# Kernel tuning notes

Measured on AMD Instinct MI355X. Metric: run time of the kernel, lower is better.

The kernel has to match this reference:

```python
import jax, jax.numpy as jnp
import numpy as np

N_NODES = 262144
MEM_DIM = 512
MSG_DIM = 1024
N_UPD = 65536


def setup_inputs() -> dict:
    key = jax.random.key(0)
    ks = jax.random.split(key, 8)
    memory = jax.random.normal(ks[0], (N_NODES, MEM_DIM), dtype=jnp.float32)
    last_update = jnp.zeros((N_NODES,), dtype=jnp.float32)
    # unique node ids (in-place scatter assumes no duplicates)
    node_ids = jax.random.permutation(ks[1], N_NODES)[:N_UPD].astype(jnp.int64)
    messages = jax.random.normal(ks[2], (N_UPD, MSG_DIM), dtype=jnp.float32)
    timestamps = jax.random.uniform(ks[3], (N_UPD,), dtype=jnp.float32)
    s_ih = 1.0 / np.sqrt(MEM_DIM)
    W_ih = jax.random.normal(ks[4], (3 * MEM_DIM, MSG_DIM), dtype=jnp.float32) * s_ih
    W_hh = jax.random.normal(ks[5], (3 * MEM_DIM, MEM_DIM), dtype=jnp.float32) * s_ih
    b_ih = jnp.zeros((3 * MEM_DIM,), dtype=jnp.float32)
    b_hh = jnp.zeros((3 * MEM_DIM,), dtype=jnp.float32)
    return {"memory": memory, "last_update": last_update, "node_ids": node_ids,
            "messages": messages, "timestamps": timestamps,
            "W_ih": W_ih, "W_hh": W_hh, "b_ih": b_ih, "b_hh": b_hh}


def gru_cell(x, h, W_ih, W_hh, b_ih, b_hh):
    # torch.nn.GRUCell semantics
    gi = x @ W_ih.T + b_ih  # [n, 3H]
    gh = h @ W_hh.T + b_hh  # [n, 3H]
    i_r, i_z, i_n = jnp.split(gi, 3, axis=-1)
    h_r, h_z, h_n = jnp.split(gh, 3, axis=-1)
    r = jax.nn.sigmoid(i_r + h_r)
    z = jax.nn.sigmoid(i_z + h_z)
    n = jnp.tanh(i_n + r * h_n)
    return (1.0 - z) * n + z * h


def reference(memory, last_update, node_ids, messages, timestamps, W_ih, W_hh, b_ih, b_hh):
    # get_updated_memory: gather -> GRU cell -> scatter back into a copy
    h = memory[node_ids]  # [n_upd, MEM_DIM]
    h_new = gru_cell(messages, h, W_ih, W_hh, b_ih, b_hh)
    updated_memory = memory.at[node_ids].set(h_new)
    updated_last_update = last_update.at[node_ids].set(timestamps)
    return updated_memory, updated_last_update
```

## Files before the change

kernel.cpp:

```cpp
#include <hip/hip_runtime.h>

#define N_NODES 262144
#define MEM_DIM 512
#define MSG_DIM 1024
#define N_UPD   65536

typedef __attribute__((ext_vector_type(8)))  __bf16 bf16x8;
typedef __attribute__((ext_vector_type(16))) float  floatx16;
typedef __attribute__((ext_vector_type(4)))  unsigned short ushortx4;

static __device__ __forceinline__ unsigned short f2bf(float f) {
  unsigned int u = __float_as_uint(f);
  u += 0x7fffu + ((u >> 16) & 1u);
  return (unsigned short)(u >> 16);
}

static __device__ __forceinline__ void async16(const void* g, void* l) {
  __builtin_amdgcn_global_load_lds(
      (const __attribute__((address_space(1))) unsigned int*)g,
      (__attribute__((address_space(3))) unsigned int*)l, 16, 0, 0);
}

__global__ void cvt_kernel(const float4* __restrict__ src,
                           ushortx4* __restrict__ dst, int n4) {
  int stride = gridDim.x * blockDim.x;
  for (int i = blockIdx.x * blockDim.x + threadIdx.x; i < n4; i += stride) {
    float4 v = src[i];
    ushortx4 o;
    o.x = f2bf(v.x); o.y = f2bf(v.y); o.z = f2bf(v.z); o.w = f2bf(v.w);
    dst[i] = o;
  }
}

__global__ void gather_cvt_kernel(const float* __restrict__ memory,
                                  const int* __restrict__ ids,
                                  ushortx4* __restrict__ dst) {
  int u = blockIdx.x * blockDim.x + threadIdx.x;
  int i = u >> 7, c4 = u & 127;
  int g = ids[i];
  const float4* row = (const float4*)(memory + (size_t)g * MEM_DIM);
  float4 v = row[c4];
  ushortx4 o;
  o.x = f2bf(v.x); o.y = f2bf(v.y); o.z = f2bf(v.z); o.w = f2bf(v.w);
  dst[u] = o;
}

__global__ void copy_kernel(const float4* __restrict__ mem,
                            const float4* __restrict__ lu,
                            float4* __restrict__ out_mem,
                            float4* __restrict__ out_lu) {
  const int NM4 = N_NODES * MEM_DIM / 4;
  const int NL4 = N_NODES / 4;
  int stride = gridDim.x * blockDim.x;
  for (int i = blockIdx.x * blockDim.x + threadIdx.x; i < NM4 + NL4; i += stride) {
    if (i < NM4) out_mem[i] = mem[i];
    else         out_lu[i - NM4] = lu[i - NM4];
  }
}

__global__ __launch_bounds__(256, 2)
void gru_kernel(const unsigned short* __restrict__ msgb,
                const unsigned short* __restrict__ hb,
                const unsigned short* __restrict__ wih,
                const unsigned short* __restrict__ whh,
                const float* __restrict__ b_ih, const float* __restrict__ b_hh,
                const float* __restrict__ memory,
                const int* __restrict__ ids,
                const float* __restrict__ ts,
                float* __restrict__ out_mem, float* __restrict__ out_lu) {
  __shared__ unsigned short sA[128 * 64];
  __shared__ unsigned short sB[192 * 64];

  const int tid  = threadIdx.x;
  const int lane = tid & 63;
  const int w    = tid >> 6;
  const int wm   = w & 1, wn = w >> 1;
  const int hc   = blockIdx.x * 64;
  const int m0   = blockIdx.y * 128;

  if (blockIdx.x == 0 && tid < 128) {
    int m = m0 + tid;
    out_lu[ids[m]] = ts[m];
  }

  floatx16 accR[2], accZ[2], accN[2][2];
#pragma unroll
  for (int t = 0; t < 2; ++t)
#pragma unroll
    for (int e = 0; e < 16; ++e) {
      accR[t][e] = 0.f; accZ[t][e] = 0.f;
      accN[0][t][e] = 0.f; accN[1][t][e] = 0.f;
    }

  const int srow = tid >> 3;
  const int scol = (tid & 7) * 8;
  const int lrow = lane & 31;
  const int lko  = (lane >> 5) * 8;

#pragma unroll
  for (int phase = 0; phase < 2; ++phase) {
    const unsigned short* Ap = phase ? hb : msgb;
    const unsigned short* Bp = phase ? whh : wih;
    const int K = phase ? 512 : 1024;
    for (int k0 = 0; k0 < K; k0 += 64) {
      __syncthreads();
#pragma unroll
      for (int j = 0; j < 4; ++j) {
        const unsigned short* g = Ap + (size_t)(m0 + j * 32 + srow) * K + (k0 + scol);
        async16(g, (char*)sA + j * 4096 + w * 1024);
      }
#pragma unroll
      for (int j = 0; j < 6; ++j) {
        int brr  = j * 32 + srow;
        int gate = brr >> 6;
        int wr   = gate * 512 + hc + (brr & 63);
        const unsigned short* g = Bp + (size_t)wr * K + (k0 + scol);
        async16(g, (char*)sB + j * 4096 + w * 1024);
      }
      __syncthreads();
#pragma unroll
      for (int kk = 0; kk < 4; ++kk) {
        int ko = kk * 16 + lko;
        bf16x8 a0 = *(const bf16x8*)&sA[(wm * 64 + lrow) * 64 + ko];
        bf16x8 a1 = *(const bf16x8*)&sA[(wm * 64 + 32 + lrow) * 64 + ko];
        bf16x8 vr = *(const bf16x8*)&sB[(wn * 32 + lrow) * 64 + ko];
        bf16x8 vz = *(const bf16x8*)&sB[(64 + wn * 32 + lrow) * 64 + ko];
        bf16x8 vn = *(const bf16x8*)&sB[(128 + wn * 32 + lrow) * 64 + ko];
        accR[0] = __builtin_amdgcn_mfma_f32_32x32x16_bf16(a0, vr, accR[0], 0, 0, 0);
        accR[1] = __builtin_amdgcn_mfma_f32_32x32x16_bf16(a1, vr, accR[1], 0, 0, 0);
        accZ[0] = __builtin_amdgcn_mfma_f32_32x32x16_bf16(a0, vz, accZ[0], 0, 0, 0);
        accZ[1] = __builtin_amdgcn_mfma_f32_32x32x16_bf16(a1, vz, accZ[1], 0, 0, 0);
        accN[phase][0] = __builtin_amdgcn_mfma_f32_32x32x16_bf16(a0, vn, accN[phase][0], 0, 0, 0);
        accN[phase][1] = __builtin_amdgcn_mfma_f32_32x32x16_bf16(a1, vn, accN[phase][1], 0, 0, 0);
      }
    }
  }

  const int col = hc + wn * 32 + lrow;
  const float biasR  = b_ih[col] + b_hh[col];
  const float biasZ  = b_ih[512 + col] + b_hh[512 + col];
  const float biasNi = b_ih[1024 + col];
  const float biasNh = b_hh[1024 + col];
#pragma unroll
  for (int t = 0; t < 2; ++t) {
#pragma unroll
    for (int r = 0; r < 16; ++r) {
      int rowin = (r & 3) + 8 * (r >> 2) + 4 * (lane >> 5);
      int m = m0 + wm * 64 + t * 32 + rowin;
      int g = ids[m];
      size_t off = (size_t)g * MEM_DIM + col;
      float h  = memory[off];
      float rr = __builtin_amdgcn_rcpf(1.f + __expf(-(accR[t][r] + biasR)));
      float zz = __builtin_amdgcn_rcpf(1.f + __expf(-(accZ[t][r] + biasZ)));
      float ni = accN[0][t][r] + biasNi;
      float hn = accN[1][t][r] + biasNh;
      float e  = __expf(2.f * (ni + rr * hn));
      float nn = 1.f - 2.f * __builtin_amdgcn_rcpf(e + 1.f);
      out_mem[off] = (1.f - zz) * nn + zz * h;
    }
  }
}

extern "C" void kernel_launch(void* const* d_in, const int* in_sizes, int n_in,
                              void* d_out, int out_size, void* d_ws, size_t ws_size,
                              hipStream_t stream) {
  const float* memory      = (const float*)d_in[0];
  const float* last_update = (const float*)d_in[1];
  const int*   node_ids    = (const int*)d_in[2];
  const float* messages    = (const float*)d_in[3];
  const float* timestamps  = (const float*)d_in[4];
  const float* W_ih        = (const float*)d_in[5];
  const float* W_hh        = (const float*)d_in[6];
  const float* b_ih        = (const float*)d_in[7];
  const float* b_hh        = (const float*)d_in[8];

  float* out_mem = (float*)d_out;
  float* out_lu  = out_mem + (size_t)N_NODES * MEM_DIM;

  char* ws = (char*)d_ws;
  unsigned short* wihb = (unsigned short*)ws;
  unsigned short* whhb = (unsigned short*)(ws + 3145728);
  unsigned short* msgb = (unsigned short*)(ws + 4718592);
  unsigned short* hb   = (unsigned short*)(ws + 138936320);

  cvt_kernel<<<1536, 256, 0, stream>>>((const float4*)W_ih, (ushortx4*)wihb, 1536 * 1024 / 4);
  cvt_kernel<<<768, 256, 0, stream>>>((const float4*)W_hh, (ushortx4*)whhb, 1536 * 512 / 4);
  cvt_kernel<<<16384, 256, 0, stream>>>((const float4*)messages, (ushortx4*)msgb, (int)((size_t)N_UPD * MSG_DIM / 4));
  gather_cvt_kernel<<<32768, 256, 0, stream>>>(memory, node_ids, (ushortx4*)hb);
  copy_kernel<<<32768, 256, 0, stream>>>((const float4*)memory, (const float4*)last_update,
                                         (float4*)d_out, (float4*)out_lu);
  gru_kernel<<<dim3(8, 512), 256, 0, stream>>>(msgb, hb, wihb, whhb, b_ih, b_hh,
                                               memory, node_ids, timestamps, out_mem, out_lu);
}
```

Before: 1.636 ms.

## Fuse copy, gather and convert passes with inverse-index map; swizzle LDS and grid

Builds an inverse node-id map so a single streaming pass over memory copies the rows that are not updated (with nontemporal stores) and converts the updated rows into the bf16 hidden buffer, which removes the separate gather pass and avoids writing rows the GRU will overwrite. Message conversion and the last_update copy are folded into the same kernel, and the weight conversions are merged into one prep kernel, cutting launches. The GRU kernel gains an XOR swizzle on LDS columns to avoid bank conflicts, a block-id swizzle so blocks sharing an M tile run together for L2 reuse, and nontemporal output stores. The added cost is a global map that must be reset on every call and an extra indirect read per row.

```diff
diff --git a/kernel.cpp b/kernel.cpp
--- a/kernel.cpp
+++ b/kernel.cpp
@@ -7,7 +7,10 @@
 
 typedef __attribute__((ext_vector_type(8)))  __bf16 bf16x8;
 typedef __attribute__((ext_vector_type(16))) float  floatx16;
+typedef __attribute__((ext_vector_type(4)))  float  floatx4;
 typedef __attribute__((ext_vector_type(4)))  unsigned short ushortx4;
+
+__device__ __align__(16) int g_inv[N_NODES];
 
 static __device__ __forceinline__ unsigned short f2bf(float f) {
   unsigned int u = __float_as_uint(f);
@@ -15,46 +18,63 @@
   return (unsigned short)(u >> 16);
 }
 
+static __device__ __forceinline__ ushortx4 cvt4(float4 v) {
+  ushortx4 o;
+  o.x = f2bf(v.x); o.y = f2bf(v.y); o.z = f2bf(v.z); o.w = f2bf(v.w);
+  return o;
+}
+
 static __device__ __forceinline__ void async16(const void* g, void* l) {
   __builtin_amdgcn_global_load_lds(
       (const __attribute__((address_space(1))) unsigned int*)g,
       (__attribute__((address_space(3))) unsigned int*)l, 16, 0, 0);
 }
 
-__global__ void cvt_kernel(const float4* __restrict__ src,
-                           ushortx4* __restrict__ dst, int n4) {
+__global__ void prep_kernel(const float4* __restrict__ wih_f, ushortx4* __restrict__ wihb,
+                            const float4* __restrict__ whh_f, ushortx4* __restrict__ whhb) {
+  const int NI4 = N_NODES / 4;
+  const int NW1 = 3 * MEM_DIM * MSG_DIM / 4;
+  const int NW2 = 3 * MEM_DIM * MEM_DIM / 4;
+  int4* inv4 = (int4*)g_inv;
   int stride = gridDim.x * blockDim.x;
-  for (int i = blockIdx.x * blockDim.x + threadIdx.x; i < n4; i += stride) {
-    float4 v = src[i];
-    ushortx4 o;
-    o.x = f2bf(v.x); o.y = f2bf(v.y); o.z = f2bf(v.z); o.w = f2bf(v.w);
-    dst[i] = o;
-  }
-}
-
-__global__ void gather_cvt_kernel(const float* __restrict__ memory,
-                                  const int* __restrict__ ids,
-                                  ushortx4* __restrict__ dst) {
+  for (int i = blockIdx.x * blockDim.x + threadIdx.x; i < NI4 + NW1 + NW2; i += stride) {
+    if (i < NI4) inv4[i] = make_int4(-1, -1, -1, -1);
+    else if (i < NI4 + NW1) { int j = i - NI4; wihb[j] = cvt4(wih_f[j]); }
+    else { int j = i - NI4 - NW1; whhb[j] = cvt4(whh_f[j]); }
+  }
+}
+
+__global__ void scatter_kernel(const int* __restrict__ ids,
+                               const float* __restrict__ ts, float* __restrict__ out_lu) {
   int u = blockIdx.x * blockDim.x + threadIdx.x;
-  int i = u >> 7, c4 = u & 127;
-  int g = ids[i];
-  const float4* row = (const float4*)(memory + (size_t)g * MEM_DIM);
-  float4 v = row[c4];
-  ushortx4 o;
-  o.x = f2bf(v.x); o.y = f2bf(v.y); o.z = f2bf(v.z); o.w = f2bf(v.w);
-  dst[u] = o;
-}
-
-__global__ void copy_kernel(const float4* __restrict__ mem,
-                            const float4* __restrict__ lu,
-                            float4* __restrict__ out_mem,
-                            float4* __restrict__ out_lu) {
+  int g = ids[u];
+  g_inv[g] = u;
+  out_lu[g] = ts[u];
+}
+
+__global__ void mega_kernel(const float4* __restrict__ mem, const float* __restrict__ lu,
+                            const float4* __restrict__ msg,
+                            float4* __restrict__ out_mem, float* __restrict__ out_lu,
+                            ushortx4* __restrict__ hb4, ushortx4* __restrict__ msgb4) {
   const int NM4 = N_NODES * MEM_DIM / 4;
-  const int NL4 = N_NODES / 4;
+  const int NG4 = N_UPD * MSG_DIM / 4;
   int stride = gridDim.x * blockDim.x;
-  for (int i = blockIdx.x * blockDim.x + threadIdx.x; i < NM4 + NL4; i += stride) {
-    if (i < NM4) out_mem[i] = mem[i];
-    else         out_lu[i - NM4] = lu[i - NM4];
+  for (int i = blockIdx.x * blockDim.x + threadIdx.x; i < NM4 + NG4 + N_NODES; i += stride) {
+    if (i < NM4) {
+      int row = i >> 7;
+      int iv = g_inv[row];
+      float4 v = mem[i];
+      if (iv < 0)
+        __builtin_nontemporal_store(*(const floatx4*)&v, (floatx4*)&out_mem[i]);
+      else
+        hb4[((size_t)iv << 7) + (i & 127)] = cvt4(v);
+    } else if (i < NM4 + NG4) {
+      int j = i - NM4;
+      msgb4[j] = cvt4(msg[j]);
+    } else {
+      int j = i - NM4 - NG4;
+      if (g_inv[j] < 0) out_lu[j] = lu[j];
+    }
   }
 }
 
@@ -66,8 +86,7 @@
                 const float* __restrict__ b_ih, const float* __restrict__ b_hh,
                 const float* __restrict__ memory,
                 const int* __restrict__ ids,
-                const float* __restrict__ ts,
-                float* __restrict__ out_mem, float* __restrict__ out_lu) {
+                float* __restrict__ out_mem) {
   __shared__ unsigned short sA[128 * 64];
   __shared__ unsigned short sB[192 * 64];
 
@@ -75,13 +94,11 @@
   const int lane = tid & 63;
   const int w    = tid >> 6;
   const int wm   = w & 1, wn = w >> 1;
-  const int hc   = blockIdx.x * 64;
-  const int m0   = blockIdx.y * 128;
-
-  if (blockIdx.x == 0 && tid < 128) {
-    int m = m0 + tid;
-    out_lu[ids[m]] = ts[m];
-  }
+
+  const int bid = blockIdx.x;
+  const int swz = (bid & 7) * 512 + (bid >> 3);
+  const int hc  = (swz & 7) * 64;
+  const int m0  = (swz >> 3) * 128;
 
   floatx16 accR[2], accZ[2], accN[2][2];
 #pragma unroll
@@ -93,9 +110,10 @@
     }
 
   const int srow = tid >> 3;
-  const int scol = (tid & 7) * 8;
+  const int scol = (((tid & 7) ^ (srow & 7)) << 3);
   const int lrow = lane & 31;
   const int lko  = (lane >> 5) * 8;
+  const int ksw  = (lrow & 7) << 3;
 
 #pragma unroll
   for (int phase = 0; phase < 2; ++phase) {
@@ -120,12 +138,12 @@
       __syncthreads();
 #pragma unroll
       for (int kk = 0; kk < 4; ++kk) {
-        int ko = kk * 16 + lko;
-        bf16x8 a0 = *(const bf16x8*)&sA[(wm * 64 + lrow) * 64 + ko];
-        bf16x8 a1 = *(const bf16x8*)&sA[(wm * 64 + 32 + lrow) * 64 + ko];
-        bf16x8 vr = *(const bf16x8*)&sB[(wn * 32 + lrow) * 64 + ko];
-        bf16x8 vz = *(const bf16x8*)&sB[(64 + wn * 32 + lrow) * 64 + ko];
-        bf16x8 vn = *(const bf16x8*)&sB[(128 + wn * 32 + lrow) * 64 + ko];
+        int kos = (kk * 16 + lko) ^ ksw;
+        bf16x8 a0 = *(const bf16x8*)&sA[(wm * 64 + lrow) * 64 + kos];
+        bf16x8 a1 = *(const bf16x8*)&sA[(wm * 64 + 32 + lrow) * 64 + kos];
+        bf16x8 vr = *(const bf16x8*)&sB[(wn * 32 + lrow) * 64 + kos];
+        bf16x8 vz = *(const bf16x8*)&sB[(64 + wn * 32 + lrow) * 64 + kos];
+        bf16x8 vn = *(const bf16x8*)&sB[(128 + wn * 32 + lrow) * 64 + kos];
         accR[0] = __builtin_amdgcn_mfma_f32_32x32x16_bf16(a0, vr, accR[0], 0, 0, 0);
         accR[1] = __builtin_amdgcn_mfma_f32_32x32x16_bf16(a1, vr, accR[1], 0, 0, 0);
         accZ[0] = __builtin_amdgcn_mfma_f32_32x32x16_bf16(a0, vz, accZ[0], 0, 0, 0);
@@ -156,7 +174,7 @@
       float hn = accN[1][t][r] + biasNh;
       float e  = __expf(2.f * (ni + rr * hn));
       float nn = 1.f - 2.f * __builtin_amdgcn_rcpf(e + 1.f);
-      out_mem[off] = (1.f - zz) * nn + zz * h;
+      __builtin_nontemporal_store((1.f - zz) * nn + zz * h, &out_mem[off]);
     }
   }
 }
@@ -183,12 +201,13 @@
   unsigned short* msgb = (unsigned short*)(ws + 4718592);
   unsigned short* hb   = (unsigned short*)(ws + 138936320);
 
-  cvt_kernel<<<1536, 256, 0, stream>>>((const float4*)W_ih, (ushortx4*)wihb, 1536 * 1024 / 4);
-  cvt_kernel<<<768, 256, 0, stream>>>((const float4*)W_hh, (ushortx4*)whhb, 1536 * 512 / 4);
-  cvt_kernel<<<16384, 256, 0, stream>>>((const float4*)messages, (ushortx4*)msgb, (int)((size_t)N_UPD * MSG_DIM / 4));
-  gather_cvt_kernel<<<32768, 256, 0, stream>>>(memory, node_ids, (ushortx4*)hb);
-  copy_kernel<<<32768, 256, 0, stream>>>((const float4*)memory, (const float4*)last_update,
-                                         (float4*)d_out, (float4*)out_lu);
-  gru_kernel<<<dim3(8, 512), 256, 0, stream>>>(msgb, hb, wihb, whhb, b_ih, b_hh,
-                                               memory, node_ids, timestamps, out_mem, out_lu);
-}
+  prep_kernel<<<1024, 256, 0, stream>>>((const float4*)W_ih, (ushortx4*)wihb,
+                                        (const float4*)W_hh, (ushortx4*)whhb);
+  scatter_kernel<<<N_UPD / 256, 256, 0, stream>>>(node_ids, timestamps, out_lu);
+  mega_kernel<<<4096, 256, 0, stream>>>((const float4*)memory, last_update,
+                                        (const float4*)messages,
+                                        (float4*)out_mem, out_lu,
+                                        (ushortx4*)hb, (ushortx4*)msgb);
+  gru_kernel<<<4096, 256, 0, stream>>>(msgb, hb, wihb, whhb, b_ih, b_hh,
+                                       memory, node_ids, out_mem);
+}
```

After: 1.415 ms. 13.5% less time.
